# Kernel tuning notes

Hardware: AMD Instinct MI355X
Metric: run time of the kernel (lower is better)

The kernel has to match this reference:

```python
import jax, jax.numpy as jnp
import numpy as np

HEADS = 4
EPS = 1e-5


def _ln(x, g, b):
    m = jnp.mean(x, axis=-1, keepdims=True)
    v = jnp.mean((x - m) ** 2, axis=-1, keepdims=True)
    return (x - m) * jax.lax.rsqrt(v + EPS) * g + b


def _gcn(x, A, W, b):
    # x: [B,N,T,C]; A: [N,N]; W: [C_out, 3C] (1x1 conv); order-2 k-hop propagation
    h = jnp.transpose(x, (0, 3, 1, 2))            # [B,C,N,T]
    h1 = jnp.einsum('bcnt,nm->bcmt', h, A)        # 1-hop
    h2 = jnp.einsum('bcnt,nm->bcmt', h1, A)       # 2-hop
    cat = jnp.concatenate([h, h1, h2], axis=1)    # [B,3C,N,T]
    out = jnp.einsum('bcnt,oc->bont', cat, W) + b[None, :, None, None]
    return jnp.transpose(out, (0, 2, 3, 1))       # [B,N,T,C_out]


def setup_inputs() -> dict:
    key = jax.random.key(0)
    ks = jax.random.split(key, 16)
    B, N, T, H = 8, 2048, 1, 64
    s = 0.02
    return {
        'query': jax.random.normal(ks[0], (B, N, T, H), jnp.float32),
        'adj': jax.random.uniform(ks[1], (N, N), jnp.float32) / N,
        'WF': jax.random.normal(ks[2], (H, 3 * H), jnp.float32) * s,
        'bF': jnp.zeros((H,), jnp.float32),
        'WD': jax.random.normal(ks[3], (H, 3 * H), jnp.float32) * s,
        'bD': jnp.zeros((H,), jnp.float32),
        'ffw1': jax.random.normal(ks[4], (6 * H, H), jnp.float32) * s,
        'ffb1': jnp.zeros((6 * H,), jnp.float32),
        'ffw2': jax.random.normal(ks[5], (H, 6 * H), jnp.float32) * s,
        'ffb2': jnp.zeros((H,), jnp.float32),
        'wq': jax.random.normal(ks[6], (H, H), jnp.float32) * s,
        'wk': jax.random.normal(ks[7], (H, H), jnp.float32) * s,
        'wv': jax.random.normal(ks[8], (H, H), jnp.float32) * s,
        'wo': jax.random.normal(ks[9], (H, H), jnp.float32) * s,
        'bo': jnp.zeros((H,), jnp.float32),
        'g2': jnp.ones((H,), jnp.float32),
        'be2': jnp.zeros((H,), jnp.float32),
        'g3': jnp.ones((H,), jnp.float32),
        'be3': jnp.zeros((H,), jnp.float32),
        'f1w': jax.random.normal(ks[10], (4 * H, H), jnp.float32) * s,
        'f1b': jnp.zeros((4 * H,), jnp.float32),
        'f2w': jax.random.normal(ks[11], (H, 4 * H), jnp.float32) * s,
        'f2b': jnp.zeros((H,), jnp.float32),
    }


def reference(query, adj, WF, bF, WD, bD, ffw1, ffb1, ffw2, ffb2,
              wq, wk, wv, wo, bo, g2, be2, g3, be3, f1w, f1b, f2w, f2b):
    B, N, T, H = query.shape
    dh = H // HEADS
    # fixed-adjacency GCN branch
    X_F = _gcn(query, adj, WF, bF)
    # dynamic adjacency
    R = query.reshape(B, N, T * H)
    R = R @ ffw1.T + ffb1
    R = R @ ffw2.T + ffb2
    R = R.sum(axis=0)                              # [N,H]
    A = R @ R.T                                    # [N,N]
    Rm = jax.nn.relu(jax.nn.softmax(A, axis=-1)) + jnp.eye(N, dtype=A.dtype)
    X_D = _gcn(query, Rm, WD, bD)
    # gated fusion
    X_DF = jnp.tanh(X_D) * jax.nn.sigmoid(X_F)     # [B,N,T,H]
    # spatial multi-head attention over N
    def heads_split(x, w):
        return jnp.transpose((x @ w.T).reshape(B, N, T, HEADS, dh), (0, 3, 2, 1, 4))
    q = heads_split(X_DF, wq)                      # [B,h,T,N,dh]
    k = heads_split(X_DF, wk)
    v = heads_split(X_DF, wv)
    scores = jnp.einsum('bhtnd,bhtmd->bhtnm', q, k) / np.sqrt(dh)
    attn = jax.nn.softmax(scores, axis=-1)
    ctx = jnp.einsum('bhtnm,bhtmd->bhtnd', attn, v)
    ctx = jnp.transpose(ctx, (0, 3, 2, 1, 4)).reshape(B, N, T, H)
    att_out = ctx @ wo.T + bo
    x = _ln(att_out + X_DF, g2, be2)
    ffn = jax.nn.relu(x @ f1w.T + f1b) @ f2w.T + f2b
    return _ln(ffn + x, g3, be3)
```

## Files before the change

kernel.cpp:

```cpp
#include <hip/hip_runtime.h>
#include <math.h>

#define NN 2048
#define BB 8
#define HD 64

typedef __attribute__((ext_vector_type(8))) short bf16x8;
typedef __attribute__((ext_vector_type(4))) float f32x4;
typedef __attribute__((ext_vector_type(16))) float f32x16;
typedef __attribute__((ext_vector_type(4))) unsigned short ushortx4;
typedef unsigned short ushort_t;

static __device__ __forceinline__ float wsum64(float v) {
#pragma unroll
    for (int off = 32; off >= 1; off >>= 1) v += __shfl_xor(v, off);
    return v;
}
static __device__ __forceinline__ float wmax64(float v) {
#pragma unroll
    for (int off = 32; off >= 1; off >>= 1) v = fmaxf(v, __shfl_xor(v, off));
    return v;
}
static __device__ __forceinline__ unsigned short brne(float x) {
    unsigned u = __float_as_uint(x);
    return (unsigned short)((u + 0x7fffu + ((u >> 16) & 1u)) >> 16);
}

#define QSCL 0.36067376022224085f

__global__ void k_prep(const float* __restrict__ ffw1, const float* __restrict__ ffb1,
                       const float* __restrict__ ffw2, const float* __restrict__ ffb2,
                       const float* __restrict__ WF, const float* __restrict__ WD,
                       const float* __restrict__ wq, const float* __restrict__ wk,
                       const float* __restrict__ wv, const float* __restrict__ wo,
                       const float* __restrict__ f1w, const float* __restrict__ f2w,
                       float* __restrict__ Wc, float* __restrict__ bc,
                       ushort_t* __restrict__ Wfb, ushort_t* __restrict__ Wdb,
                       ushort_t* __restrict__ Wqkvb, ushort_t* __restrict__ wob,
                       ushort_t* __restrict__ f1wb, ushort_t* __restrict__ f2wb) {
    int idx = blockIdx.x * 256 + threadIdx.x;
    if (idx < 4096) {
        int o = idx >> 6, c = idx & 63;
        float s = 0.f;
        for (int j = 0; j < 384; ++j) s += ffw2[o * 384 + j] * ffw1[j * 64 + c];
        Wc[idx] = s;
        wob[idx] = brne(wo[idx]);
    }
    if (idx < 64) {
        float s = ffb2[idx];
        for (int j = 0; j < 384; ++j) s += ffw2[idx * 384 + j] * ffb1[j];
        bc[idx] = s;
    }
    if (idx < 12288) {
        Wfb[idx] = brne(WF[idx]);
        Wdb[idx] = brne(WD[idx]);
        int o = idx >> 6, c = idx & 63;
        float v = o < 64 ? wq[o * 64 + c] * QSCL
                         : (o < 128 ? wk[(o - 64) * 64 + c] : wv[(o - 128) * 64 + c]);
        Wqkvb[idx] = brne(v);
    }
    if (idx < 16384) {
        f1wb[idx] = brne(f1w[idx]);
        f2wb[idx] = brne(f2w[idx]);
    }
}

__global__ __launch_bounds__(256) void k_qprep(const float* __restrict__ q,
                                               float* __restrict__ Qcat,
                                               ushort_t* __restrict__ Qcatb,
                                               float* __restrict__ Qsum) {
    int idx = blockIdx.x * 256 + threadIdx.x;
    int n = idx >> 6, c = idx & 63;
    float s = 0.f;
#pragma unroll
    for (int b = 0; b < BB; ++b) {
        float v = q[((size_t)b * NN + n) * 64 + c];
        s += v;
        Qcat[(size_t)n * 512 + b * 64 + c] = v;
        Qcatb[(size_t)n * 512 + b * 64 + c] = brne(v);
    }
    Qsum[idx] = s;
}

__global__ __launch_bounds__(256) void k_rsum(const float* __restrict__ Qsum,
                                              const float* __restrict__ Wc,
                                              const float* __restrict__ bc,
                                              ushort_t* __restrict__ Rsumb) {
    __shared__ float W[64][65];
    int tid = threadIdx.x;
    for (int i = tid; i < 4096; i += 256) W[i >> 6][i & 63] = Wc[i];
    __syncthreads();
    int idx = blockIdx.x * 256 + tid;
    int n = idx >> 6, h = idx & 63;
    const float* qs = &Qsum[n * 64];
    float s = 8.f * bc[h];
    for (int c = 0; c < 64; ++c) s += qs[c] * W[h][c];
    Rsumb[idx] = brne(s);
}

__global__ __launch_bounds__(256) void k_amat_m(const ushort_t* __restrict__ Rb,
                                                float* __restrict__ A) {
    __shared__ __align__(16) ushort_t As[4096];
    __shared__ __align__(16) ushort_t Bs[4096];
    int n0 = blockIdx.y * 64, m0 = blockIdx.x * 64;
    int t = threadIdx.x;
    int srow = t >> 2, scb = (t & 3) * 2;
    int sw = srow & 7;
    const int lane = t & 63, w = t >> 6;
    const int wm = w >> 1, wj = w & 1;
    const int lg = lane >> 4, lr = lane & 15;
    const int ma = wm * 32 + lr, mb = ma + 16;
    const int ja = wj * 32 + lr, jb = ja + 16;
    const int swa = ma & 7, swb = ja & 7;
    bf16x8 g0 = *(const bf16x8*)(Rb + (size_t)(n0 + srow) * 64 + scb * 8);
    bf16x8 g1 = *(const bf16x8*)(Rb + (size_t)(n0 + srow) * 64 + scb * 8 + 8);
    bf16x8 x0 = *(const bf16x8*)(Rb + (size_t)(m0 + srow) * 64 + scb * 8);
    bf16x8 x1 = *(const bf16x8*)(Rb + (size_t)(m0 + srow) * 64 + scb * 8 + 8);
    *(bf16x8*)&As[srow * 64 + ((scb    ) ^ sw) * 8] = g0;
    *(bf16x8*)&As[srow * 64 + ((scb + 1) ^ sw) * 8] = g1;
    *(bf16x8*)&Bs[srow * 64 + ((scb    ) ^ sw) * 8] = x0;
    *(bf16x8*)&Bs[srow * 64 + ((scb + 1) ^ sw) * 8] = x1;
    __syncthreads();
    f32x4 acc00 = {}, acc01 = {}, acc10 = {}, acc11 = {};
#pragma unroll
    for (int kk = 0; kk < 2; ++kk) {
        int c = kk * 4 + lg;
        bf16x8 a0 = *(const bf16x8*)&As[ma * 64 + (c ^ swa) * 8];
        bf16x8 a1 = *(const bf16x8*)&As[mb * 64 + (c ^ swa) * 8];
        bf16x8 b0 = *(const bf16x8*)&Bs[ja * 64 + (c ^ swb) * 8];
        bf16x8 b1 = *(const bf16x8*)&Bs[jb * 64 + (c ^ swb) * 8];
        acc00 = __builtin_amdgcn_mfma_f32_16x16x32_bf16(a0, b0, acc00, 0, 0, 0);
        acc01 = __builtin_amdgcn_mfma_f32_16x16x32_bf16(a0, b1, acc01, 0, 0, 0);
        acc10 = __builtin_amdgcn_mfma_f32_16x16x32_bf16(a1, b0, acc10, 0, 0, 0);
        acc11 = __builtin_amdgcn_mfma_f32_16x16x32_bf16(a1, b1, acc11, 0, 0, 0);
    }
    int jA = m0 + wj * 32 + lr;
    int nA = n0 + wm * 32 + lg * 4;
#pragma unroll
    for (int r = 0; r < 4; ++r) {
        A[(size_t)(nA + r) * NN + jA]           = acc00[r];
        A[(size_t)(nA + r) * NN + jA + 16]      = acc01[r];
        A[(size_t)(nA + 16 + r) * NN + jA]      = acc10[r];
        A[(size_t)(nA + 16 + r) * NN + jA + 16] = acc11[r];
    }
}

__global__ __launch_bounds__(256) void k_softmax(float* __restrict__ A) {
    __shared__ float red[8];
    int n = blockIdx.x, tid = threadIdx.x;
    float4* row = (float4*)&A[(size_t)n * NN];
    float4 a = row[tid * 2], b = row[tid * 2 + 1];
    float v[8] = {a.x, a.y, a.z, a.w, b.x, b.y, b.z, b.w};
    float mx = v[0];
#pragma unroll
    for (int i = 1; i < 8; ++i) mx = fmaxf(mx, v[i]);
    mx = wmax64(mx);
    int wid = tid >> 6, lane = tid & 63;
    if (lane == 0) red[wid] = mx;
    __syncthreads();
    mx = fmaxf(fmaxf(red[0], red[1]), fmaxf(red[2], red[3]));
    float s = 0.f;
#pragma unroll
    for (int i = 0; i < 8; ++i) { v[i] = exp2f((v[i] - mx) * 1.44269504f); s += v[i]; }
    s = wsum64(s);
    if (lane == 0) red[4 + wid] = s;
    __syncthreads();
    s = red[4] + red[5] + red[6] + red[7];
    float inv = 1.f / s;
    int col = tid * 8;
#pragma unroll
    for (int i = 0; i < 8; ++i) v[i] = v[i] * inv + ((col + i) == n ? 1.f : 0.f);
    row[tid * 2]     = make_float4(v[0], v[1], v[2], v[3]);
    row[tid * 2 + 1] = make_float4(v[4], v[5], v[6], v[7]);
}

__global__ __launch_bounds__(256) void k_t32to16(const float* __restrict__ in,
                                                 ushort_t* __restrict__ out,
                                                 int R, int C) {
    __shared__ float tile[64][65];
    int r0 = blockIdx.y * 64, c0 = blockIdx.x * 64;
    int t = threadIdx.x;
    int tr = t >> 6, tc = t & 63;
#pragma unroll
    for (int i = 0; i < 16; ++i) {
        int r = tr + i * 4;
        tile[r][tc] = in[(size_t)(r0 + r) * C + c0 + tc];
    }
    __syncthreads();
#pragma unroll
    for (int i = 0; i < 16; ++i) {
        int cc = tr + i * 4;
        out[(size_t)(c0 + cc) * R + r0 + tc] = brne(tile[tc][cc]);
    }
}

__global__ __launch_bounds__(256) void k_hop(const ushort_t* __restrict__ G0t,
                                             const ushort_t* __restrict__ G1t,
                                             const ushort_t* __restrict__ B0t,
                                             const ushort_t* __restrict__ B1t,
                                             float* __restrict__ Y0, float* __restrict__ Y1,
                                             ushort_t* __restrict__ T0, ushort_t* __restrict__ T1,
                                             ushort_t* __restrict__ R0, ushort_t* __restrict__ R1) {
    __shared__ __align__(16) ushort_t As[4096];
    __shared__ __align__(16) ushort_t Bs[4096];
    int z = blockIdx.z;
    const ushort_t* Gt = z ? G1t : G0t;
    const ushort_t* Xt = z ? B1t : B0t;
    float* Y = z ? Y1 : Y0;
    ushort_t* T = z ? T1 : T0;
    ushort_t* R = z ? R1 : R0;
    int m0 = blockIdx.y * 64, j0 = blockIdx.x * 64;
    int t = threadIdx.x;
    int srow = t >> 2, scb = (t & 3) * 2;
    int sw = srow & 7;
    const int lane = t & 63, w = t >> 6;
    const int wm = w >> 1, wj = w & 1;
    const int lg = lane >> 4, lr = lane & 15;
    const int ma = wm * 32 + lr, mb = ma + 16;
    const int ja = wj * 32 + lr, jb = ja + 16;
    const int swa = ma & 7, swb = ja & 7;
    f32x4 acc00 = {}, acc01 = {}, acc10 = {}, acc11 = {};
    const size_t gbase = (size_t)(m0 + srow) * NN;
    const size_t xbase = (size_t)(j0 + srow) * NN;
    for (int k0 = 0; k0 < NN; k0 += 64) {
        bf16x8 g0 = *(const bf16x8*)(Gt + gbase + k0 + scb * 8);
        bf16x8 g1 = *(const bf16x8*)(Gt + gbase + k0 + scb * 8 + 8);
        bf16x8 x0 = *(const bf16x8*)(Xt + xbase + k0 + scb * 8);
        bf16x8 x1 = *(const bf16x8*)(Xt + xbase + k0 + scb * 8 + 8);
        __syncthreads();
        *(bf16x8*)&As[srow * 64 + ((scb    ) ^ sw) * 8] = g0;
        *(bf16x8*)&As[srow * 64 + ((scb + 1) ^ sw) * 8] = g1;
        *(bf16x8*)&Bs[srow * 64 + ((scb    ) ^ sw) * 8] = x0;
        *(bf16x8*)&Bs[srow * 64 + ((scb + 1) ^ sw) * 8] = x1;
        __syncthreads();
#pragma unroll
        for (int kk = 0; kk < 2; ++kk) {
            int c = kk * 4 + lg;
            bf16x8 a0 = *(const bf16x8*)&As[ma * 64 + (c ^ swa) * 8];
            bf16x8 a1 = *(const bf16x8*)&As[mb * 64 + (c ^ swa) * 8];
            bf16x8 b0 = *(const bf16x8*)&Bs[ja * 64 + (c ^ swb) * 8];
            bf16x8 b1 = *(const bf16x8*)&Bs[jb * 64 + (c ^ swb) * 8];
            acc00 = __builtin_amdgcn_mfma_f32_16x16x32_bf16(a0, b0, acc00, 0, 0, 0);
            acc01 = __builtin_amdgcn_mfma_f32_16x16x32_bf16(a0, b1, acc01, 0, 0, 0);
            acc10 = __builtin_amdgcn_mfma_f32_16x16x32_bf16(a1, b0, acc10, 0, 0, 0);
            acc11 = __builtin_amdgcn_mfma_f32_16x16x32_bf16(a1, b1, acc11, 0, 0, 0);
        }
    }
    int jA = j0 + wj * 32 + lr;
    int mA = m0 + wm * 32 + lg * 4;
    if (Y) {
#pragma unroll
        for (int r = 0; r < 4; ++r) {
            Y[(size_t)(mA + r) * 512 + jA]           = acc00[r];
            Y[(size_t)(mA + r) * 512 + jA + 16]      = acc01[r];
            Y[(size_t)(mA + 16 + r) * 512 + jA]      = acc10[r];
            Y[(size_t)(mA + 16 + r) * 512 + jA + 16] = acc11[r];
        }
    }
    if (T || R) {
        ushortx4 p0, p1, p2, p3;
#pragma unroll
        for (int r = 0; r < 4; ++r) {
            p0[r] = brne(acc00[r]);
            p1[r] = brne(acc01[r]);
            p2[r] = brne(acc10[r]);
            p3[r] = brne(acc11[r]);
        }
        if (T) {
            *(ushortx4*)&T[(size_t)jA * NN + mA]             = p0;
            *(ushortx4*)&T[(size_t)(jA + 16) * NN + mA]      = p1;
            *(ushortx4*)&T[(size_t)jA * NN + mA + 16]        = p2;
            *(ushortx4*)&T[(size_t)(jA + 16) * NN + mA + 16] = p3;
        }
        if (R) {
#pragma unroll
            for (int r = 0; r < 4; ++r) {
                R[(size_t)(mA + r) * 512 + jA]           = p0[r];
                R[(size_t)(mA + r) * 512 + jA + 16]      = p1[r];
                R[(size_t)(mA + 16 + r) * 512 + jA]      = p2[r];
                R[(size_t)(mA + 16 + r) * 512 + jA + 16] = p3[r];
            }
        }
    }
}

__global__ __launch_bounds__(256) void k_gcnz(const ushort_t* __restrict__ Qcatb,
                                              const ushort_t* __restrict__ X1Fb,
                                              const ushort_t* __restrict__ X2Fb,
                                              const ushort_t* __restrict__ X1Db,
                                              const ushort_t* __restrict__ X2Db,
                                              const ushort_t* __restrict__ Wfb,
                                              const ushort_t* __restrict__ Wdb,
                                              const float* __restrict__ bF,
                                              const float* __restrict__ bD,
                                              float* __restrict__ XDF,
                                              ushort_t* __restrict__ XDFb) {
    __shared__ ushort_t Wl[2][64][200];
    int tid = threadIdx.x;
    for (int i = tid; i < 12288; i += 256) {
        int o = i / 192, k = i % 192;
        Wl[0][o][k] = Wfb[i];
        Wl[1][o][k] = Wdb[i];
    }
    int blk = blockIdx.x;
    int b = blk >> 5, n0 = (blk & 31) * 64;
    int lane = tid & 63, rt = tid >> 6;
    int lr = lane & 15, lg = lane >> 4;
    int nA = n0 + rt * 16 + lr;
    const size_t rb = (size_t)nA * 512 + b * 64 + lg * 8;
    bf16x8 aQ0  = *(const bf16x8*)(Qcatb + rb);
    bf16x8 aQ1  = *(const bf16x8*)(Qcatb + rb + 32);
    bf16x8 a1F0 = *(const bf16x8*)(X1Fb + rb);
    bf16x8 a1F1 = *(const bf16x8*)(X1Fb + rb + 32);
    bf16x8 a2F0 = *(const bf16x8*)(X2Fb + rb);
    bf16x8 a2F1 = *(const bf16x8*)(X2Fb + rb + 32);
    bf16x8 a1D0 = *(const bf16x8*)(X1Db + rb);
    bf16x8 a1D1 = *(const bf16x8*)(X1Db + rb + 32);
    bf16x8 a2D0 = *(const bf16x8*)(X2Db + rb);
    bf16x8 a2D1 = *(const bf16x8*)(X2Db + rb + 32);
    float bFv[4], bDv[4];
#pragma unroll
    for (int ot = 0; ot < 4; ++ot) { bFv[ot] = bF[ot * 16 + lr]; bDv[ot] = bD[ot * 16 + lr]; }
    __syncthreads();
    f32x4 accF[4], accD[4];
#pragma unroll
    for (int ot = 0; ot < 4; ++ot) {
        int o = ot * 16 + lr;
        const ushort_t* wf = &Wl[0][o][lg * 8];
        const ushort_t* wd = &Wl[1][o][lg * 8];
        f32x4 aF = {}, aD = {};
        aF = __builtin_amdgcn_mfma_f32_16x16x32_bf16(aQ0,  *(const bf16x8*)(wf),       aF, 0, 0, 0);
        aF = __builtin_amdgcn_mfma_f32_16x16x32_bf16(aQ1,  *(const bf16x8*)(wf + 32),  aF, 0, 0, 0);
        aF = __builtin_amdgcn_mfma_f32_16x16x32_bf16(a1F0, *(const bf16x8*)(wf + 64),  aF, 0, 0, 0);
        aF = __builtin_amdgcn_mfma_f32_16x16x32_bf16(a1F1, *(const bf16x8*)(wf + 96),  aF, 0, 0, 0);
        aF = __builtin_amdgcn_mfma_f32_16x16x32_bf16(a2F0, *(const bf16x8*)(wf + 128), aF, 0, 0, 0);
        aF = __builtin_amdgcn_mfma_f32_16x16x32_bf16(a2F1, *(const bf16x8*)(wf + 160), aF, 0, 0, 0);
        aD = __builtin_amdgcn_mfma_f32_16x16x32_bf16(aQ0,  *(const bf16x8*)(wd),       aD, 0, 0, 0);
        aD = __builtin_amdgcn_mfma_f32_16x16x32_bf16(aQ1,  *(const bf16x8*)(wd + 32),  aD, 0, 0, 0);
        aD = __builtin_amdgcn_mfma_f32_16x16x32_bf16(a1D0, *(const bf16x8*)(wd + 64),  aD, 0, 0, 0);
        aD = __builtin_amdgcn_mfma_f32_16x16x32_bf16(a1D1, *(const bf16x8*)(wd + 96),  aD, 0, 0, 0);
        aD = __builtin_amdgcn_mfma_f32_16x16x32_bf16(a2D0, *(const bf16x8*)(wd + 128), aD, 0, 0, 0);
        aD = __builtin_amdgcn_mfma_f32_16x16x32_bf16(a2D1, *(const bf16x8*)(wd + 160), aD, 0, 0, 0);
        accF[ot] = aF; accD[ot] = aD;
    }
    const float L2E = 1.44269504f;
#pragma unroll
    for (int ot = 0; ot < 4; ++ot) {
#pragma unroll
        for (int r = 0; r < 4; ++r) {
            float f = accF[ot][r] + bFv[ot];
            float d = accD[ot][r] + bDv[ot];
            float sg = 1.f / (1.f + exp2f(-f * L2E));
            float th = 2.f / (1.f + exp2f(-2.f * d * L2E)) - 1.f;
            float xv = th * sg;
            int nD = n0 + rt * 16 + lg * 4 + r;
            size_t oa = ((size_t)b * NN + nD) * 64 + ot * 16 + lr;
            XDF[oa] = xv;
            XDFb[oa] = brne(xv);
        }
    }
}

__global__ __launch_bounds__(256) void k_qkvm(const ushort_t* __restrict__ XDFb,
                                              const ushort_t* __restrict__ Wqkvb,
                                              ushort_t* __restrict__ qb,
                                              ushort_t* __restrict__ kb,
                                              ushort_t* __restrict__ vbt) {
    __shared__ ushort_t Wl[192][72];
    __shared__ float vt[4][64][17];
    int tid = threadIdx.x;
    for (int i = tid; i < 12288; i += 256) Wl[i >> 6][i & 63] = Wqkvb[i];
    int blk = blockIdx.x;
    size_t row0 = (size_t)blk * 64;
    int b = (int)(row0 >> 11), nbase = (int)(row0 & 2047);
    int lane = tid & 63, rt = tid >> 6;
    int lr = lane & 15, lg = lane >> 4;
    int nl = rt * 16 + lr;
    const ushort_t* xr = XDFb + (row0 + nl) * 64 + lg * 8;
    bf16x8 a0 = *(const bf16x8*)(xr);
    bf16x8 a1 = *(const bf16x8*)(xr + 32);
    __syncthreads();
#pragma unroll
    for (int ot = 0; ot < 12; ++ot) {
        f32x4 acc = {};
        const ushort_t* wp = &Wl[ot * 16 + lr][lg * 8];
        acc = __builtin_amdgcn_mfma_f32_16x16x32_bf16(a0, *(const bf16x8*)(wp),      acc, 0, 0, 0);
        acc = __builtin_amdgcn_mfma_f32_16x16x32_bf16(a1, *(const bf16x8*)(wp + 32), acc, 0, 0, 0);
        int kind = ot >> 2, h = ot & 3;
        int nD = rt * 16 + lg * 4;
        if (kind < 2) {
            ushort_t* dst = (kind == 0 ? qb : kb) + (((size_t)(b * 4 + h) * NN + nbase + nD) * 16 + lr);
#pragma unroll
            for (int r = 0; r < 4; ++r) dst[r * 16] = brne(acc[r]);
        } else {
#pragma unroll
            for (int r = 0; r < 4; ++r) vt[h][nD + r][lr] = acc[r];
        }
    }
    __syncthreads();
    if (tid < 128) {
        int h = tid >> 5, d = (tid >> 1) & 15, half = tid & 1;
        ushort_t* dst = vbt + ((size_t)(b * 4 + h) * 32 + d) * NN + nbase + half * 32;
#pragma unroll
        for (int g = 0; g < 4; ++g) {
            uint4 u;
            int i0 = half * 32 + g * 8;
            u.x = (unsigned)brne(vt[h][i0 + 0][d]) | ((unsigned)brne(vt[h][i0 + 1][d]) << 16);
            u.y = (unsigned)brne(vt[h][i0 + 2][d]) | ((unsigned)brne(vt[h][i0 + 3][d]) << 16);
            u.z = (unsigned)brne(vt[h][i0 + 4][d]) | ((unsigned)brne(vt[h][i0 + 5][d]) << 16);
            u.w = (unsigned)brne(vt[h][i0 + 6][d]) | ((unsigned)brne(vt[h][i0 + 7][d]) << 16);
            ((uint4*)dst)[g] = u;
        }
    } else {
        int t2 = tid - 128;
        int h = t2 >> 5, dz = 16 + ((t2 >> 1) & 15), half = t2 & 1;
        unsigned pv = (dz == 16) ? 0x3F803F80u : 0u;
        uint4 z; z.x = pv; z.y = pv; z.z = pv; z.w = pv;
        ushort_t* dst = vbt + ((size_t)(b * 4 + h) * 32 + dz) * NN + nbase + half * 32;
#pragma unroll
        for (int g = 0; g < 4; ++g) ((uint4*)dst)[g] = z;
    }
}

__global__ __launch_bounds__(256) void k_attn_mf(const ushort_t* __restrict__ qb,
                                                 const ushort_t* __restrict__ kb,
                                                 const ushort_t* __restrict__ vbt,
                                                 ushort_t* __restrict__ ctx) {
    __shared__ float cpart[4][32][33];
    int bh = blockIdx.y, n0 = blockIdx.x * 64;
    int tid = threadIdx.x, w = tid >> 6, l = tid & 63;
    int lc = l & 31, hi = l >> 5;
    int qsub = w & 1, mhalf = w >> 1;
    const ushort_t* Q  = qb + ((size_t)bh * NN + n0 + qsub * 32) * 16;
    const ushort_t* K  = kb + (size_t)bh * NN * 16;
    const ushort_t* VT = vbt + ((size_t)bh * 32 + lc) * NN;
    bf16x8 qf = *(const bf16x8*)(Q + lc * 16 + hi * 8);
    f32x16 zero = {};
    f32x16 acc = {};
    for (int m0 = mhalf * 32; m0 < NN; m0 += 64) {
        bf16x8 kf = *(const bf16x8*)(K + (size_t)(m0 + lc) * 16 + hi * 8);
        bf16x8 v0 = *(const bf16x8*)(VT + m0 + hi * 8);
        bf16x8 v1 = *(const bf16x8*)(VT + m0 + 16 + hi * 8);
        f32x16 st = __builtin_amdgcn_mfma_f32_32x32x16_bf16(kf, qf, zero, 0, 0, 0);
        float p[16];
#pragma unroll
        for (int r = 0; r < 16; ++r) p[r] = exp2f(st[r]);
        unsigned d[8];
#pragma unroll
        for (int j = 0; j < 8; ++j)
            asm("v_cvt_pk_bf16_f32 %0, %1, %2" : "=v"(d[j]) : "v"(p[2 * j]), "v"(p[2 * j + 1]));
        unsigned z0 = hi ? d[0] : d[2];
        unsigned z1 = hi ? d[1] : d[3];
        unsigned z2 = hi ? d[4] : d[6];
        unsigned z3 = hi ? d[5] : d[7];
        unsigned r0 = (unsigned)__shfl_xor((int)z0, 32);
        unsigned r1 = (unsigned)__shfl_xor((int)z1, 32);
        unsigned r2 = (unsigned)__shfl_xor((int)z2, 32);
        unsigned r3 = (unsigned)__shfl_xor((int)z3, 32);
        union { bf16x8 v; unsigned u[4]; } fa, fb;
        if (hi == 0) {
            fa.u[0] = d[0]; fa.u[1] = d[1]; fa.u[2] = r0; fa.u[3] = r1;
            fb.u[0] = d[4]; fb.u[1] = d[5]; fb.u[2] = r2; fb.u[3] = r3;
        } else {
            fa.u[0] = r0; fa.u[1] = r1; fa.u[2] = d[2]; fa.u[3] = d[3];
            fb.u[0] = r2; fb.u[1] = r3; fb.u[2] = d[6]; fb.u[3] = d[7];
        }
        acc = __builtin_amdgcn_mfma_f32_32x32x16_bf16(fa.v, v0, acc, 0, 0, 0);
        acc = __builtin_amdgcn_mfma_f32_32x32x16_bf16(fb.v, v1, acc, 0, 0, 0);
    }
#pragma unroll
    for (int r = 0; r < 16; ++r)
        cpart[w][(r & 3) + 8 * (r >> 2) + 4 * hi][lc] = acc[r];
    __syncthreads();
    int q = tid >> 2, d4 = (tid & 3) * 4;
    int qs = q >> 5, q32 = q & 31;
    float sst = cpart[qs][q32][16] + cpart[2 + qs][q32][16];
    float inv = 1.f / sst;
    ushortx4 ob;
    ob[0] = brne((cpart[qs][q32][d4]     + cpart[2 + qs][q32][d4])     * inv);
    ob[1] = brne((cpart[qs][q32][d4 + 1] + cpart[2 + qs][q32][d4 + 1]) * inv);
    ob[2] = brne((cpart[qs][q32][d4 + 2] + cpart[2 + qs][q32][d4 + 2]) * inv);
    ob[3] = brne((cpart[qs][q32][d4 + 3] + cpart[2 + qs][q32][d4 + 3]) * inv);
    int b = bh >> 2, h = bh & 3;
    *(ushortx4*)&ctx[((size_t)b * NN + n0 + q) * 64 + h * 16 + d4] = ob;
}

__global__ __launch_bounds__(256) void k_tail(const ushort_t* __restrict__ ctxb,
                                              const float* __restrict__ XDF,
                                              const ushort_t* __restrict__ wob,
                                              const float* __restrict__ bo,
                                              const float* __restrict__ g2,
                                              const float* __restrict__ be2,
                                              const ushort_t* __restrict__ f1wb,
                                              const float* __restrict__ f1b,
                                              const ushort_t* __restrict__ f2wb,
                                              const float* __restrict__ f2b,
                                              const float* __restrict__ g3,
                                              const float* __restrict__ be3,
                                              float* __restrict__ out) {
    __shared__ ushort_t xs[64][72];
    __shared__ ushort_t tl[64][264];
    int tid = threadIdx.x;
    size_t row0 = (size_t)blockIdx.x * 64;
    int lane = tid & 63, rt = tid >> 6;
    int lr = lane & 15, lg = lane >> 4;
    const ushort_t* cr = ctxb + (row0 + rt * 16 + lr) * 64 + lg * 8;
    bf16x8 c0 = *(const bf16x8*)(cr);
    bf16x8 c1 = *(const bf16x8*)(cr + 32);
    f32x4 acc1[4];
#pragma unroll
    for (int ot = 0; ot < 4; ++ot) {
        f32x4 a = {};
        const ushort_t* wp = wob + (size_t)(ot * 16 + lr) * 64 + lg * 8;
        a = __builtin_amdgcn_mfma_f32_16x16x32_bf16(c0, *(const bf16x8*)(wp),      a, 0, 0, 0);
        a = __builtin_amdgcn_mfma_f32_16x16x32_bf16(c1, *(const bf16x8*)(wp + 32), a, 0, 0, 0);
        acc1[ot] = a;
    }
    float bov[4], g2v[4], be2v[4];
#pragma unroll
    for (int ot = 0; ot < 4; ++ot) {
        int ch = ot * 16 + lr;
        bov[ot] = bo[ch]; g2v[ot] = g2[ch]; be2v[ot] = be2[ch];
    }
    float x1k[4][4];
#pragma unroll
    for (int r = 0; r < 4; ++r) {
        int rowL = rt * 16 + lg * 4 + r;
        float y[4]; float s = 0.f;
#pragma unroll
        for (int ot = 0; ot < 4; ++ot) {
            y[ot] = acc1[ot][r] + bov[ot] + XDF[(row0 + rowL) * 64 + ot * 16 + lr];
            s += y[ot];
        }
        s += __shfl_xor(s, 1); s += __shfl_xor(s, 2);
        s += __shfl_xor(s, 4); s += __shfl_xor(s, 8);
        float mean = s * (1.f / 64.f);
        float vs = 0.f;
#pragma unroll
        for (int ot = 0; ot < 4; ++ot) { float dd = y[ot] - mean; vs += dd * dd; }
        vs += __shfl_xor(vs, 1); vs += __shfl_xor(vs, 2);
        vs += __shfl_xor(vs, 4); vs += __shfl_xor(vs, 8);
        float rstd = rsqrtf(vs * (1.f / 64.f) + 1e-5f);
#pragma unroll
        for (int ot = 0; ot < 4; ++ot) {
            float v = (y[ot] - mean) * rstd * g2v[ot] + be2v[ot];
            x1k[r][ot] = v;
            xs[rowL][ot * 16 + lr] = brne(v);
        }
    }
    __syncthreads();
    bf16x8 a0 = *(const bf16x8*)&xs[rt * 16 + lr][lg * 8];
    bf16x8 a1 = *(const bf16x8*)&xs[rt * 16 + lr][32 + lg * 8];
#pragma unroll
    for (int jt = 0; jt < 16; ++jt) {
        f32x4 acc = {};
        const ushort_t* wp = f1wb + (size_t)(jt * 16 + lr) * 64 + lg * 8;
        acc = __builtin_amdgcn_mfma_f32_16x16x32_bf16(a0, *(const bf16x8*)(wp),      acc, 0, 0, 0);
        acc = __builtin_amdgcn_mfma_f32_16x16x32_bf16(a1, *(const bf16x8*)(wp + 32), acc, 0, 0, 0);
        float bj = f1b[jt * 16 + lr];
#pragma unroll
        for (int r = 0; r < 4; ++r)
            tl[rt * 16 + lg * 4 + r][jt * 16 + lr] = brne(fmaxf(acc[r] + bj, 0.f));
    }
    __syncthreads();
    bf16x8 af[8];
#pragma unroll
    for (int kc = 0; kc < 8; ++kc)
        af[kc] = *(const bf16x8*)&tl[rt * 16 + lr][kc * 32 + lg * 8];
    f32x4 acc2[4];
#pragma unroll
    for (int ot = 0; ot < 4; ++ot) {
        f32x4 a = {};
#pragma unroll
        for (int kc = 0; kc < 8; ++kc) {
            bf16x8 bf = *(const bf16x8*)(f2wb + (size_t)(ot * 16 + lr) * 256 + kc * 32 + lg * 8);
            a = __builtin_amdgcn_mfma_f32_16x16x32_bf16(af[kc], bf, a, 0, 0, 0);
        }
        acc2[ot] = a;
    }
    float g3v[4], be3v[4], f2bv[4];
#pragma unroll
    for (int ot = 0; ot < 4; ++ot) {
        int o = ot * 16 + lr;
        g3v[ot] = g3[o]; be3v[ot] = be3[o]; f2bv[ot] = f2b[o];
    }
#pragma unroll
    for (int r = 0; r < 4; ++r) {
        int rowL = rt * 16 + lg * 4 + r;
        float y[4]; float s = 0.f;
#pragma unroll
        for (int ot = 0; ot < 4; ++ot) {
            y[ot] = acc2[ot][r] + f2bv[ot] + x1k[r][ot];
            s += y[ot];
        }
        s += __shfl_xor(s, 1); s += __shfl_xor(s, 2);
        s += __shfl_xor(s, 4); s += __shfl_xor(s, 8);
        float mean = s * (1.f / 64.f);
        float vs = 0.f;
#pragma unroll
        for (int ot = 0; ot < 4; ++ot) { float dd = y[ot] - mean; vs += dd * dd; }
        vs += __shfl_xor(vs, 1); vs += __shfl_xor(vs, 2);
        vs += __shfl_xor(vs, 4); vs += __shfl_xor(vs, 8);
        float rstd = rsqrtf(vs * (1.f / 64.f) + 1e-5f);
#pragma unroll
        for (int ot = 0; ot < 4; ++ot)
            out[(row0 + rowL) * 64 + ot * 16 + lr] = (y[ot] - mean) * rstd * g3v[ot] + be3v[ot];
    }
}

extern "C" void kernel_launch(void* const* d_in, const int* in_sizes, int n_in,
                              void* d_out, int out_size, void* d_ws, size_t ws_size,
                              hipStream_t stream) {
    const float* query = (const float*)d_in[0];
    const float* adj   = (const float*)d_in[1];
    const float* WF    = (const float*)d_in[2];
    const float* bF    = (const float*)d_in[3];
    const float* WD    = (const float*)d_in[4];
    const float* bD    = (const float*)d_in[5];
    const float* ffw1  = (const float*)d_in[6];
    const float* ffb1  = (const float*)d_in[7];
    const float* ffw2  = (const float*)d_in[8];
    const float* ffb2  = (const float*)d_in[9];
    const float* wq    = (const float*)d_in[10];
    const float* wk    = (const float*)d_in[11];
    const float* wv    = (const float*)d_in[12];
    const float* wo    = (const float*)d_in[13];
    const float* bo    = (const float*)d_in[14];
    const float* g2    = (const float*)d_in[15];
    const float* be2   = (const float*)d_in[16];
    const float* g3    = (const float*)d_in[17];
    const float* be3   = (const float*)d_in[18];
    const float* f1w   = (const float*)d_in[19];
    const float* f1b   = (const float*)d_in[20];
    const float* f2w   = (const float*)d_in[21];
    const float* f2b   = (const float*)d_in[22];
    float* out = (float*)d_out;

    float* w = (float*)d_ws;
    float*    Qcat  = w;
    float*    Qsum  = w + 1048576;
    float*    Wc    = w + 1179648;
    float*    bc    = w + 1183744;
    ushort_t* Wfb   = (ushort_t*)(w + 1184000);
    ushort_t* Wdb   = (ushort_t*)(w + 1190144);
    ushort_t* Wqkvb = (ushort_t*)(w + 1196288);
    ushort_t* f1wb  = (ushort_t*)(w + 1202432);
    ushort_t* f2wb  = (ushort_t*)(w + 1210624);
    ushort_t* Rsumb = (ushort_t*)(w + 1218816);
    ushort_t* wob   = (ushort_t*)(w + 1284352);
    float*    Amat  = w + 1349888;
    ushort_t* adjT  = (ushort_t*)(w + 5544192);
    ushort_t* RmT   = (ushort_t*)(w + 7641344);
    ushort_t* QcatT = (ushort_t*)(w + 9738496);
    ushort_t* Qcatb = (ushort_t*)(w + 10262784);
    ushort_t* X1FT  = (ushort_t*)(w + 10787072);
    ushort_t* X1DT  = (ushort_t*)(w + 11311360);
    ushort_t* X1Fb  = (ushort_t*)(w + 11835648);
    ushort_t* X1Db  = (ushort_t*)(w + 12359936);
    ushort_t* X2Db  = (ushort_t*)(w + 12884224);
    ushort_t* X2Fb  = QcatT;
    ushort_t* qb    = (ushort_t*)Qcat;
    ushort_t* kb    = (ushort_t*)(Qcat + 524288);
    ushort_t* vbt   = (ushort_t*)Amat;
    ushort_t* ctxb  = (ushort_t*)(Amat + 1048576);
    float*    XDF   = (float*)adjT;
    ushort_t* XDFb  = RmT;

    k_prep<<<64, 256, 0, stream>>>(ffw1, ffb1, ffw2, ffb2, WF, WD, wq, wk, wv, wo, f1w, f2w,
                                   Wc, bc, Wfb, Wdb, Wqkvb, wob, f1wb, f2wb);
    k_qprep<<<512, 256, 0, stream>>>(query, Qcat, Qcatb, Qsum);
    k_rsum<<<512, 256, 0, stream>>>(Qsum, Wc, bc, Rsumb);
    k_amat_m<<<dim3(32, 32), 256, 0, stream>>>(Rsumb, Amat);
    k_softmax<<<2048, 256, 0, stream>>>(Amat);

    k_t32to16<<<dim3(32, 32), 256, 0, stream>>>(adj, adjT, NN, NN);
    k_t32to16<<<dim3(32, 32), 256, 0, stream>>>(Amat, RmT, NN, NN);
    k_t32to16<<<dim3(8, 32), 256, 0, stream>>>(Qcat, QcatT, NN, 512);

    k_hop<<<dim3(8, 32, 2), 256, 0, stream>>>(adjT, RmT, QcatT, QcatT,
                                              nullptr, nullptr, X1FT, X1DT, X1Fb, X1Db);
    k_hop<<<dim3(8, 32, 2), 256, 0, stream>>>(adjT, RmT, X1FT, X1DT,
                                              nullptr, nullptr, nullptr, nullptr, X2Fb, X2Db);

    k_gcnz<<<256, 256, 0, stream>>>(Qcatb, X1Fb, X2Fb, X1Db, X2Db, Wfb, Wdb, bF, bD,
                                    XDF, XDFb);
    k_qkvm<<<256, 256, 0, stream>>>(XDFb, Wqkvb, qb, kb, vbt);
    k_attn_mf<<<dim3(32, 32), 256, 0, stream>>>(qb, kb, vbt, ctxb);
    k_tail<<<256, 256, 0, stream>>>(ctxb, XDF, wob, bo, g2, be2,
                                    f1wb, f1b, f2wb, f2b, g3, be3, out);
}
```

Before: 292.3 us.

## Split attention keys across two blocks, prefetch hop tiles, fuse rsum into qprep

The attention kernel now splits the key dimension in two (grid z=2). Each half writes an unnormalized bf16 partial context and its softmax denominator, and the tail kernel combines the halves and normalizes them before the output projection. This doubles the attention block count to improve occupancy. The hop GEMM register-prefetches the next k-tile's global loads so they overlap the MFMA work, and its unused fp32 output path is removed. The rsum projection is fused into qprep, which drops one launch and the Qsum round trip. Risks: the split assumes a shared max or no max subtraction across halves, the partials lose precision from bf16 rounding before normalization, and the tail does extra combining work.

```diff
diff --git a/kernel.cpp b/kernel.cpp
--- a/kernel.cpp
+++ b/kernel.cpp
@@ -68,9 +68,15 @@
 __global__ __launch_bounds__(256) void k_qprep(const float* __restrict__ q,
                                                float* __restrict__ Qcat,
                                                ushort_t* __restrict__ Qcatb,
-                                               float* __restrict__ Qsum) {
-    int idx = blockIdx.x * 256 + threadIdx.x;
-    int n = idx >> 6, c = idx & 63;
+                                               const float* __restrict__ Wc,
+                                               const float* __restrict__ bc,
+                                               ushort_t* __restrict__ Rsumb) {
+    __shared__ float W[64][65];
+    __shared__ float qsum[4][64];
+    int tid = threadIdx.x;
+    for (int i = tid; i < 4096; i += 256) W[i >> 6][i & 63] = Wc[i];
+    int nl = tid >> 6, c = tid & 63;
+    int n = blockIdx.x * 4 + nl;
     float s = 0.f;
 #pragma unroll
     for (int b = 0; b < BB; ++b) {
@@ -79,23 +85,13 @@
         Qcat[(size_t)n * 512 + b * 64 + c] = v;
         Qcatb[(size_t)n * 512 + b * 64 + c] = brne(v);
     }
-    Qsum[idx] = s;
-}
-
-__global__ __launch_bounds__(256) void k_rsum(const float* __restrict__ Qsum,
-                                              const float* __restrict__ Wc,
-                                              const float* __restrict__ bc,
-                                              ushort_t* __restrict__ Rsumb) {
-    __shared__ float W[64][65];
-    int tid = threadIdx.x;
-    for (int i = tid; i < 4096; i += 256) W[i >> 6][i & 63] = Wc[i];
-    __syncthreads();
-    int idx = blockIdx.x * 256 + tid;
-    int n = idx >> 6, h = idx & 63;
-    const float* qs = &Qsum[n * 64];
-    float s = 8.f * bc[h];
-    for (int c = 0; c < 64; ++c) s += qs[c] * W[h][c];
-    Rsumb[idx] = brne(s);
+    qsum[nl][c] = s;
+    __syncthreads();
+    int h = c;
+    float r = 8.f * bc[h];
+    const float* qs = qsum[nl];
+    for (int c2 = 0; c2 < 64; ++c2) r += qs[c2] * W[h][c2];
+    Rsumb[n * 64 + h] = brne(r);
 }
 
 __global__ __launch_bounds__(256) void k_amat_m(const ushort_t* __restrict__ Rb,
@@ -198,7 +194,6 @@
                                              const ushort_t* __restrict__ G1t,
                                              const ushort_t* __restrict__ B0t,
                                              const ushort_t* __restrict__ B1t,
-                                             float* __restrict__ Y0, float* __restrict__ Y1,
                                              ushort_t* __restrict__ T0, ushort_t* __restrict__ T1,
                                              ushort_t* __restrict__ R0, ushort_t* __restrict__ R1) {
     __shared__ __align__(16) ushort_t As[4096];
@@ -206,7 +201,6 @@
     int z = blockIdx.z;
     const ushort_t* Gt = z ? G1t : G0t;
     const ushort_t* Xt = z ? B1t : B0t;
-    float* Y = z ? Y1 : Y0;
     ushort_t* T = z ? T1 : T0;
     ushort_t* R = z ? R1 : R0;
     int m0 = blockIdx.y * 64, j0 = blockIdx.x * 64;
@@ -220,19 +214,24 @@
     const int ja = wj * 32 + lr, jb = ja + 16;
     const int swa = ma & 7, swb = ja & 7;
     f32x4 acc00 = {}, acc01 = {}, acc10 = {}, acc11 = {};
-    const size_t gbase = (size_t)(m0 + srow) * NN;
-    const size_t xbase = (size_t)(j0 + srow) * NN;
+    const ushort_t* Gp = Gt + (size_t)(m0 + srow) * NN + scb * 8;
+    const ushort_t* Xp = Xt + (size_t)(j0 + srow) * NN + scb * 8;
+    bf16x8 g0 = *(const bf16x8*)(Gp);
+    bf16x8 g1 = *(const bf16x8*)(Gp + 8);
+    bf16x8 x0 = *(const bf16x8*)(Xp);
+    bf16x8 x1 = *(const bf16x8*)(Xp + 8);
     for (int k0 = 0; k0 < NN; k0 += 64) {
-        bf16x8 g0 = *(const bf16x8*)(Gt + gbase + k0 + scb * 8);
-        bf16x8 g1 = *(const bf16x8*)(Gt + gbase + k0 + scb * 8 + 8);
-        bf16x8 x0 = *(const bf16x8*)(Xt + xbase + k0 + scb * 8);
-        bf16x8 x1 = *(const bf16x8*)(Xt + xbase + k0 + scb * 8 + 8);
         __syncthreads();
         *(bf16x8*)&As[srow * 64 + ((scb    ) ^ sw) * 8] = g0;
         *(bf16x8*)&As[srow * 64 + ((scb + 1) ^ sw) * 8] = g1;
         *(bf16x8*)&Bs[srow * 64 + ((scb    ) ^ sw) * 8] = x0;
         *(bf16x8*)&Bs[srow * 64 + ((scb + 1) ^ sw) * 8] = x1;
         __syncthreads();
+        int kn = (k0 + 64) & (NN - 1);
+        g0 = *(const bf16x8*)(Gp + kn);
+        g1 = *(const bf16x8*)(Gp + kn + 8);
+        x0 = *(const bf16x8*)(Xp + kn);
+        x1 = *(const bf16x8*)(Xp + kn + 8);
 #pragma unroll
         for (int kk = 0; kk < 2; ++kk) {
             int c = kk * 4 + lg;
@@ -248,38 +247,27 @@
     }
     int jA = j0 + wj * 32 + lr;
     int mA = m0 + wm * 32 + lg * 4;
-    if (Y) {
+    ushortx4 p0, p1, p2, p3;
+#pragma unroll
+    for (int r = 0; r < 4; ++r) {
+        p0[r] = brne(acc00[r]);
+        p1[r] = brne(acc01[r]);
+        p2[r] = brne(acc10[r]);
+        p3[r] = brne(acc11[r]);
+    }
+    if (T) {
+        *(ushortx4*)&T[(size_t)jA * NN + mA]             = p0;
+        *(ushortx4*)&T[(size_t)(jA + 16) * NN + mA]      = p1;
+        *(ushortx4*)&T[(size_t)jA * NN + mA + 16]        = p2;
+        *(ushortx4*)&T[(size_t)(jA + 16) * NN + mA + 16] = p3;
+    }
+    if (R) {
 #pragma unroll
         for (int r = 0; r < 4; ++r) {
-            Y[(size_t)(mA + r) * 512 + jA]           = acc00[r];
-            Y[(size_t)(mA + r) * 512 + jA + 16]      = acc01[r];
-            Y[(size_t)(mA + 16 + r) * 512 + jA]      = acc10[r];
-            Y[(size_t)(mA + 16 + r) * 512 + jA + 16] = acc11[r];
-        }
-    }
-    if (T || R) {
-        ushortx4 p0, p1, p2, p3;
-#pragma unroll
-        for (int r = 0; r < 4; ++r) {
-            p0[r] = brne(acc00[r]);
-            p1[r] = brne(acc01[r]);
-            p2[r] = brne(acc10[r]);
-            p3[r] = brne(acc11[r]);
-        }
-        if (T) {
-            *(ushortx4*)&T[(size_t)jA * NN + mA]             = p0;
-            *(ushortx4*)&T[(size_t)(jA + 16) * NN + mA]      = p1;
-            *(ushortx4*)&T[(size_t)jA * NN + mA + 16]        = p2;
-            *(ushortx4*)&T[(size_t)(jA + 16) * NN + mA + 16] = p3;
-        }
-        if (R) {
-#pragma unroll
-            for (int r = 0; r < 4; ++r) {
-                R[(size_t)(mA + r) * 512 + jA]           = p0[r];
-                R[(size_t)(mA + r) * 512 + jA + 16]      = p1[r];
-                R[(size_t)(mA + 16 + r) * 512 + jA]      = p2[r];
-                R[(size_t)(mA + 16 + r) * 512 + jA + 16] = p3[r];
-            }
+            R[(size_t)(mA + r) * 512 + jA]           = p0[r];
+            R[(size_t)(mA + r) * 512 + jA + 16]      = p1[r];
+            R[(size_t)(mA + 16 + r) * 512 + jA]      = p2[r];
+            R[(size_t)(mA + 16 + r) * 512 + jA + 16] = p3[r];
         }
     }
 }
@@ -425,9 +413,11 @@
 __global__ __launch_bounds__(256) void k_attn_mf(const ushort_t* __restrict__ qb,
                                                  const ushort_t* __restrict__ kb,
                                                  const ushort_t* __restrict__ vbt,
-                                                 ushort_t* __restrict__ ctx) {
+                                                 ushort_t* __restrict__ P0,
+                                                 ushort_t* __restrict__ P1,
+                                                 float* __restrict__ ssumA) {
     __shared__ float cpart[4][32][33];
-    int bh = blockIdx.y, n0 = blockIdx.x * 64;
+    int bh = blockIdx.y, n0 = blockIdx.x * 64, sp = blockIdx.z;
     int tid = threadIdx.x, w = tid >> 6, l = tid & 63;
     int lc = l & 31, hi = l >> 5;
     int qsub = w & 1, mhalf = w >> 1;
@@ -437,7 +427,8 @@
     bf16x8 qf = *(const bf16x8*)(Q + lc * 16 + hi * 8);
     f32x16 zero = {};
     f32x16 acc = {};
-    for (int m0 = mhalf * 32; m0 < NN; m0 += 64) {
+    int kbeg = sp * (NN / 2), kend = kbeg + NN / 2;
+    for (int m0 = kbeg + mhalf * 32; m0 < kend; m0 += 64) {
         bf16x8 kf = *(const bf16x8*)(K + (size_t)(m0 + lc) * 16 + hi * 8);
         bf16x8 v0 = *(const bf16x8*)(VT + m0 + hi * 8);
         bf16x8 v1 = *(const bf16x8*)(VT + m0 + 16 + hi * 8);
@@ -475,17 +466,21 @@
     int q = tid >> 2, d4 = (tid & 3) * 4;
     int qs = q >> 5, q32 = q & 31;
     float sst = cpart[qs][q32][16] + cpart[2 + qs][q32][16];
-    float inv = 1.f / sst;
     ushortx4 ob;
-    ob[0] = brne((cpart[qs][q32][d4]     + cpart[2 + qs][q32][d4])     * inv);
-    ob[1] = brne((cpart[qs][q32][d4 + 1] + cpart[2 + qs][q32][d4 + 1]) * inv);
-    ob[2] = brne((cpart[qs][q32][d4 + 2] + cpart[2 + qs][q32][d4 + 2]) * inv);
-    ob[3] = brne((cpart[qs][q32][d4 + 3] + cpart[2 + qs][q32][d4 + 3]) * inv);
+    ob[0] = brne(cpart[qs][q32][d4]     + cpart[2 + qs][q32][d4]);
+    ob[1] = brne(cpart[qs][q32][d4 + 1] + cpart[2 + qs][q32][d4 + 1]);
+    ob[2] = brne(cpart[qs][q32][d4 + 2] + cpart[2 + qs][q32][d4 + 2]);
+    ob[3] = brne(cpart[qs][q32][d4 + 3] + cpart[2 + qs][q32][d4 + 3]);
     int b = bh >> 2, h = bh & 3;
-    *(ushortx4*)&ctx[((size_t)b * NN + n0 + q) * 64 + h * 16 + d4] = ob;
-}
-
-__global__ __launch_bounds__(256) void k_tail(const ushort_t* __restrict__ ctxb,
+    ushort_t* P = sp ? P1 : P0;
+    *(ushortx4*)&P[((size_t)b * NN + n0 + q) * 64 + h * 16 + d4] = ob;
+    if ((tid & 3) == 0)
+        ssumA[(size_t)sp * 32 * NN + (size_t)bh * NN + n0 + q] = sst;
+}
+
+__global__ __launch_bounds__(256) void k_tail(const ushort_t* __restrict__ P0,
+                                              const ushort_t* __restrict__ P1,
+                                              const float* __restrict__ ssumA,
                                               const float* __restrict__ XDF,
                                               const ushort_t* __restrict__ wob,
                                               const float* __restrict__ bo,
@@ -504,9 +499,30 @@
     size_t row0 = (size_t)blockIdx.x * 64;
     int lane = tid & 63, rt = tid >> 6;
     int lr = lane & 15, lg = lane >> 4;
-    const ushort_t* cr = ctxb + (row0 + rt * 16 + lr) * 64 + lg * 8;
-    bf16x8 c0 = *(const bf16x8*)(cr);
-    bf16x8 c1 = *(const bf16x8*)(cr + 32);
+    {
+        int r2 = tid >> 2, hh = tid & 3;
+        size_t rowG = row0 + r2;
+        int bb = (int)(rowG >> 11), nn = (int)(rowG & 2047);
+        size_t si = (size_t)(bb * 4 + hh) * NN + nn;
+        float inv = 1.f / (ssumA[si] + ssumA[(size_t)32 * NN + si]);
+        const ushort_t* p0 = P0 + rowG * 64 + hh * 16;
+        const ushort_t* p1 = P1 + rowG * 64 + hh * 16;
+#pragma unroll
+        for (int g = 0; g < 4; ++g) {
+            ushortx4 u0 = *(const ushortx4*)(p0 + g * 4);
+            ushortx4 u1 = *(const ushortx4*)(p1 + g * 4);
+#pragma unroll
+            for (int j = 0; j < 4; ++j) {
+                float v0 = __uint_as_float((unsigned)u0[j] << 16);
+                float v1 = __uint_as_float((unsigned)u1[j] << 16);
+                xs[r2][hh * 16 + g * 4 + j] = brne((v0 + v1) * inv);
+            }
+        }
+    }
+    __syncthreads();
+    bf16x8 c0 = *(const bf16x8*)&xs[rt * 16 + lr][lg * 8];
+    bf16x8 c1 = *(const bf16x8*)&xs[rt * 16 + lr][32 + lg * 8];
+    __syncthreads();
     f32x4 acc1[4];
 #pragma unroll
     for (int ot = 0; ot < 4; ++ot) {
@@ -638,7 +654,6 @@
 
     float* w = (float*)d_ws;
     float*    Qcat  = w;
-    float*    Qsum  = w + 1048576;
     float*    Wc    = w + 1179648;
     float*    bc    = w + 1183744;
     ushort_t* Wfb   = (ushort_t*)(w + 1184000);
@@ -662,14 +677,15 @@
     ushort_t* qb    = (ushort_t*)Qcat;
     ushort_t* kb    = (ushort_t*)(Qcat + 524288);
     ushort_t* vbt   = (ushort_t*)Amat;
-    ushort_t* ctxb  = (ushort_t*)(Amat + 1048576);
+    ushort_t* P0    = (ushort_t*)(Amat + 1048576);
+    ushort_t* P1    = (ushort_t*)(Amat + 1572864);
+    float*    ssumA = Amat + 2097152;
     float*    XDF   = (float*)adjT;
     ushort_t* XDFb  = RmT;
 
     k_prep<<<64, 256, 0, stream>>>(ffw1, ffb1, ffw2, ffb2, WF, WD, wq, wk, wv, wo, f1w, f2w,
                                    Wc, bc, Wfb, Wdb, Wqkvb, wob, f1wb, f2wb);
-    k_qprep<<<512, 256, 0, stream>>>(query, Qcat, Qcatb, Qsum);
-    k_rsum<<<512, 256, 0, stream>>>(Qsum, Wc, bc, Rsumb);
+    k_qprep<<<512, 256, 0, stream>>>(query, Qcat, Qcatb, Wc, bc, Rsumb);
     k_amat_m<<<dim3(32, 32), 256, 0, stream>>>(Rsumb, Amat);
     k_softmax<<<2048, 256, 0, stream>>>(Amat);
 
@@ -678,14 +694,14 @@
     k_t32to16<<<dim3(8, 32), 256, 0, stream>>>(Qcat, QcatT, NN, 512);
 
     k_hop<<<dim3(8, 32, 2), 256, 0, stream>>>(adjT, RmT, QcatT, QcatT,
-                                              nullptr, nullptr, X1FT, X1DT, X1Fb, X1Db);
+                                              X1FT, X1DT, X1Fb, X1Db);
     k_hop<<<dim3(8, 32, 2), 256, 0, stream>>>(adjT, RmT, X1FT, X1DT,
-                                              nullptr, nullptr, nullptr, nullptr, X2Fb, X2Db);
+                                              nullptr, nullptr, X2Fb, X2Db);
 
     k_gcnz<<<256, 256, 0, stream>>>(Qcatb, X1Fb, X2Fb, X1Db, X2Db, Wfb, Wdb, bF, bD,
                                     XDF, XDFb);
     k_qkvm<<<256, 256, 0, stream>>>(XDFb, Wqkvb, qb, kb, vbt);
-    k_attn_mf<<<dim3(32, 32), 256, 0, stream>>>(qb, kb, vbt, ctxb);
-    k_tail<<<256, 256, 0, stream>>>(ctxb, XDF, wob, bo, g2, be2,
+    k_attn_mf<<<dim3(32, 32, 2), 256, 0, stream>>>(qb, kb, vbt, P0, P1, ssumA);
+    k_tail<<<256, 256, 0, stream>>>(P0, P1, ssumA, XDF, wob, bo, g2, be2,
                                     f1wb, f1b, f2wb, f2b, g3, be3, out);
 }
```

Result: no change. 289.3 us (-1.0%).
